# Optimization experiments

Measured on AMD Instinct MI355X. Metric: run time of the kernel, lower is better.

Reference implementation:

```python
import jax, jax.numpy as jnp
import numpy as np

G = 50000            # number of 5-node crystal graphs
NPG = 5              # nodes per graph (forward reshapes to (-1, 5, F))
N = G * NPG          # total nodes
IN = 64              # in_size (61 atomic-number feats + 3 position)
OUT = 64             # out_size
HID = 2 * OUT        # hidden width per __init__


def setup_inputs() -> dict:
    key = jax.random.key(0)
    ks = jax.random.split(key, 8)
    h = jax.random.normal(ks[0], (N, IN - 3), jnp.float32)
    x = jax.random.normal(ks[1], (N, 3), jnp.float32)
    # complete graph with self-loops inside each 5-node crystal
    base = np.arange(G, dtype=np.int64) * NPG
    li = np.repeat(np.arange(NPG, dtype=np.int64), NPG)
    lj = np.tile(np.arange(NPG, dtype=np.int64), NPG)
    src = jnp.asarray((base[:, None] + li[None, :]).reshape(-1))
    dst = jnp.asarray((base[:, None] + lj[None, :]).reshape(-1))

    def lin(k, fi, fo):
        return jax.random.normal(k, (fi, fo), jnp.float32) / np.float32(np.sqrt(fi))

    W1 = lin(ks[2], IN, HID);  b1 = jnp.zeros((HID,), jnp.float32)
    W2 = lin(ks[3], HID, HID); b2 = jnp.zeros((HID,), jnp.float32)
    W3 = lin(ks[4], HID, HID); b3 = jnp.zeros((HID,), jnp.float32)
    W4 = lin(ks[5], HID, OUT); b4 = jnp.zeros((OUT,), jnp.float32)
    return {"h": h, "x": x, "src": src, "dst": dst,
            "W1": W1, "b1": b1, "W2": W2, "b2": b2,
            "W3": W3, "b3": b3, "W4": W4, "b4": b4}


def _graph_conv(feat, src, dst, W, b):
    # DGL GraphConv, norm='both': D_dst^{-1/2} A D_src^{-1/2} X W + b
    e = src.shape[0]
    ones = jnp.ones((e,), feat.dtype)
    deg_out = jax.ops.segment_sum(ones, src, num_segments=N)
    deg_in = jax.ops.segment_sum(ones, dst, num_segments=N)
    norm_src = jax.lax.rsqrt(jnp.maximum(deg_out, 1.0))
    norm_dst = jax.lax.rsqrt(jnp.maximum(deg_in, 1.0))
    norm_e = norm_src[src] * norm_dst[dst]                      # [E]
    agg = jax.ops.segment_sum(feat[src] * norm_e[:, None], dst,
                              num_segments=N)                   # [N, F]
    return agg @ W + b


def reference(h, x, src, dst, W1, b1, W2, b2, W3, b3, W4, b4):
    hx = jnp.concatenate([h, x.astype(jnp.float32)], axis=1)   # [N, IN]
    f1 = _graph_conv(hx, src, dst, W1, b1)
    f2 = _graph_conv(f1, src, dst, W2, b2)
    f3 = _graph_conv(f2, src, dst, W3, b3)
    f4 = _graph_conv(f3, src, dst, W4, b4)                      # [N, OUT]
    return jnp.mean(f4.reshape((-1, NPG, f4.shape[-1])), axis=1)  # [G, OUT]
```

## Files before the change

### kernel.cpp

```cpp
#include <hip/hip_runtime.h>


#define GB 16

__global__ void __launch_bounds__(256) collapse1(
    const float* __restrict__ W1, const float* __restrict__ b1,
    const float* __restrict__ W2, const float* __restrict__ b2,
    const float* __restrict__ W3, const float* __restrict__ b3,
    const float* __restrict__ W4, const float* __restrict__ b4,
    float* __restrict__ ws) {
  __shared__ __align__(16) float smem[128 * 128 + 512];
  int tid = threadIdx.x;
  int bx = blockIdx.x;

  if (bx < 32) {
    float* W2s = smem;
    float* w1s = smem + 16384;
    int i0 = bx * 2;
    {
      const float4* s = (const float4*)W2;
      float4* d = (float4*)W2s;
      #pragma unroll
      for (int j = 0; j < 16; ++j) d[tid + 256 * j] = s[tid + 256 * j];
      if (tid < 64) ((float4*)w1s)[tid] = ((const float4*)(W1 + i0 * 128))[tid];
    }
    __syncthreads();
    int il = tid >> 7, oo = tid & 127;
    float s0 = 0.f, s1 = 0.f, s2 = 0.f, s3 = 0.f;
    #pragma unroll 8
    for (int k = 0; k < 128; k += 4) {
      s0 += w1s[il * 128 + k + 0] * W2s[(k + 0) * 128 + oo];
      s1 += w1s[il * 128 + k + 1] * W2s[(k + 1) * 128 + oo];
      s2 += w1s[il * 128 + k + 2] * W2s[(k + 2) * 128 + oo];
      s3 += w1s[il * 128 + k + 3] * W2s[(k + 3) * 128 + oo];
    }
    ws[(i0 + il) * 128 + oo] = (s0 + s1) + (s2 + s3);
    if (bx == 0 && tid < 128) {
      float s = b2[tid];
      #pragma unroll 4
      for (int k = 0; k < 128; ++k) s += b1[k] * W2s[k * 128 + tid];
      ws[16384 + tid] = s;
    }
  } else {
    float* W4s = smem;
    float* w3s = smem + 8192;
    int i0 = (bx - 32) * 4;
    {
      const float4* s = (const float4*)W4;
      float4* d = (float4*)W4s;
      #pragma unroll
      for (int j = 0; j < 8; ++j) d[tid + 256 * j] = s[tid + 256 * j];
      if (tid < 128) ((float4*)w3s)[tid] = ((const float4*)(W3 + i0 * 128))[tid];
    }
    __syncthreads();
    int il = tid >> 6, o = tid & 63;
    float s0 = 0.f, s1 = 0.f, s2 = 0.f, s3 = 0.f;
    #pragma unroll 8
    for (int k = 0; k < 128; k += 4) {
      s0 += w3s[il * 128 + k + 0] * W4s[(k + 0) * 64 + o];
      s1 += w3s[il * 128 + k + 1] * W4s[(k + 1) * 64 + o];
      s2 += w3s[il * 128 + k + 2] * W4s[(k + 2) * 64 + o];
      s3 += w3s[il * 128 + k + 3] * W4s[(k + 3) * 64 + o];
    }
    ws[8192 + (i0 + il) * 64 + o] = (s0 + s1) + (s2 + s3);
    if (bx == 32 && tid < 64) {
      float s = b4[tid];
      #pragma unroll 4
      for (int k = 0; k < 128; ++k) s += b3[k] * W4s[k * 64 + tid];
      ws[16512 + tid] = s;
    }
  }
}

__global__ void __launch_bounds__(256) collapse2(float* __restrict__ ws) {
  __shared__ __align__(16) float smem[128 * 64 + 512];
  float* Bms = smem;
  float* As  = smem + 8192;
  int tid = threadIdx.x;
  int i0 = blockIdx.x * 4;
  {
    const float4* s = (const float4*)(ws + 8192);
    float4* d = (float4*)Bms;
    #pragma unroll
    for (int j = 0; j < 8; ++j) d[tid + 256 * j] = s[tid + 256 * j];
    if (tid < 128) ((float4*)As)[tid] = ((const float4*)(ws + i0 * 128))[tid];
  }
  __syncthreads();
  int il = tid >> 6, o = tid & 63;
  float s0 = 0.f, s1 = 0.f, s2 = 0.f, s3 = 0.f;
  #pragma unroll 8
  for (int k = 0; k < 128; k += 4) {
    s0 += As[il * 128 + k + 0] * Bms[(k + 0) * 64 + o];
    s1 += As[il * 128 + k + 1] * Bms[(k + 1) * 64 + o];
    s2 += As[il * 128 + k + 2] * Bms[(k + 2) * 64 + o];
    s3 += As[il * 128 + k + 3] * Bms[(k + 3) * 64 + o];
  }
  ws[16640 + (i0 >> 2) * 256 + o * 4 + il] = ((s0 + s1) + (s2 + s3)) * 0.2f;
  if (blockIdx.x == 0 && tid < 64) {
    float s = ws[16512 + tid];
    #pragma unroll 4
    for (int k = 0; k < 128; ++k) s += ws[16384 + k] * Bms[k * 64 + tid];
    ws[20736 + tid] = s;
  }
}

__global__ void __launch_bounds__(256) gcn_main(
    const float* __restrict__ h, const float* __restrict__ x,
    const float* __restrict__ ws, float* __restrict__ out, int G) {
  __shared__ __align__(16) float m_s[4][4][64];

  int tid = threadIdx.x, wv = tid >> 6, lane = tid & 63;
  long gbase = (long)blockIdx.x * GB + wv * 4;
  if (gbase >= G) return;

  float bco = ws[20736 + lane];

  float sv[4];
  #pragma unroll
  for (int j = 0; j < 4; ++j) {
    long g = gbase + j;
    if (g < G) {
      if (lane < 61) {
        const float* p = h + g * 305 + lane;
        sv[j] = p[0] + p[61] + p[122] + p[183] + p[244];
      } else {
        const float* p = x + g * 15 + (lane - 61);
        sv[j] = p[0] + p[3] + p[6] + p[9] + p[12];
      }
    } else {
      sv[j] = 0.f;
    }
  }
  #pragma unroll
  for (int j = 0; j < 4; ++j) m_s[wv][j][lane] = sv[j];

  {
    const float4* Wg = (const float4*)(ws + 16640);
    const float4* m0 = (const float4*)&m_s[wv][0][0];
    const float4* m1 = (const float4*)&m_s[wv][1][0];
    const float4* m2 = (const float4*)&m_s[wv][2][0];
    const float4* m3 = (const float4*)&m_s[wv][3][0];
    float a0 = bco, a1 = bco, a2 = bco, a3 = bco;
    #pragma unroll 4
    for (int q = 0; q < 16; ++q) {
      float4 w = Wg[q * 64 + lane];
      float4 v0 = m0[q];
      float4 v1 = m1[q];
      float4 v2 = m2[q];
      float4 v3 = m3[q];
      a0 += v0.x * w.x + v0.y * w.y + v0.z * w.z + v0.w * w.w;
      a1 += v1.x * w.x + v1.y * w.y + v1.z * w.z + v1.w * w.w;
      a2 += v2.x * w.x + v2.y * w.y + v2.z * w.z + v2.w * w.w;
      a3 += v3.x * w.x + v3.y * w.y + v3.z * w.z + v3.w * w.w;
    }
    long ob = gbase * 64 + lane;
    if (gbase + 0 < G) out[ob + 0]   = a0;
    if (gbase + 1 < G) out[ob + 64]  = a1;
    if (gbase + 2 < G) out[ob + 128] = a2;
    if (gbase + 3 < G) out[ob + 192] = a3;
  }
}

extern "C" void kernel_launch(void* const* d_in, const int* in_sizes, int n_in,
                              void* d_out, int out_size, void* d_ws, size_t ws_size,
                              hipStream_t stream) {
  const float* h  = (const float*)d_in[0];
  const float* x  = (const float*)d_in[1];
  const float* W1 = (const float*)d_in[4];
  const float* b1 = (const float*)d_in[5];
  const float* W2 = (const float*)d_in[6];
  const float* b2 = (const float*)d_in[7];
  const float* W3 = (const float*)d_in[8];
  const float* b3 = (const float*)d_in[9];
  const float* W4 = (const float*)d_in[10];
  const float* b4 = (const float*)d_in[11];
  float* ws = (float*)d_ws;
  float* out = (float*)d_out;

  int G = in_sizes[0] / 305;

  collapse1<<<64, 256, 0, stream>>>(W1, b1, W2, b2, W3, b3, W4, b4, ws);
  collapse2<<<16, 256, 0, stream>>>(ws);

  int blocks = (G + GB - 1) / GB;
  gcn_main<<<blocks, 256, 0, stream>>>(h, x, ws, out, G);
}
```

Baseline: 38.48 us.

## Fuse weight-collapse kernels into one single-block kernel and unify gather pointer

Replaces the two weight-collapse kernels (64 and 16 blocks) with a single 1024-thread block that computes W1·W2·W3·W4 sequentially in shared memory. This removes one kernel launch and the global-memory round-trip of the intermediate products. The trade-off is that the whole chain of three 128-wide matmuls now runs serially on one CU instead of spread across many. The main kernel's gather also folds the h/x branch into one strided pointer to avoid lane divergence.

```diff
diff --git a/kernel.cpp b/kernel.cpp
--- a/kernel.cpp
+++ b/kernel.cpp
@@ -3,104 +3,125 @@
 
 #define GB 16
 
-__global__ void __launch_bounds__(256) collapse1(
+__global__ void __launch_bounds__(1024) collapse(
     const float* __restrict__ W1, const float* __restrict__ b1,
     const float* __restrict__ W2, const float* __restrict__ b2,
     const float* __restrict__ W3, const float* __restrict__ b3,
     const float* __restrict__ W4, const float* __restrict__ b4,
     float* __restrict__ ws) {
-  __shared__ __align__(16) float smem[128 * 128 + 512];
+  __shared__ __align__(16) float wbuf[128 * 128];
+  __shared__ __align__(16) float A[64 * 128];
+  __shared__ __align__(16) float T[64 * 128];
+  __shared__ float bA[128], bT[128];
   int tid = threadIdx.x;
-  int bx = blockIdx.x;
-
-  if (bx < 32) {
-    float* W2s = smem;
-    float* w1s = smem + 16384;
-    int i0 = bx * 2;
-    {
-      const float4* s = (const float4*)W2;
-      float4* d = (float4*)W2s;
-      #pragma unroll
-      for (int j = 0; j < 16; ++j) d[tid + 256 * j] = s[tid + 256 * j];
-      if (tid < 64) ((float4*)w1s)[tid] = ((const float4*)(W1 + i0 * 128))[tid];
-    }
-    __syncthreads();
-    int il = tid >> 7, oo = tid & 127;
+  int o128 = tid & 127, grp8 = tid >> 7;
+  int o64 = tid & 63,  grp16 = tid >> 6;
+
+  {
+    const float4* s = (const float4*)W2;
+    float4* d = (float4*)wbuf;
+    #pragma unroll
+    for (int r = 0; r < 4; ++r) d[tid + 1024 * r] = s[tid + 1024 * r];
+  }
+  __syncthreads();
+
+  #pragma unroll 2
+  for (int r = 0; r < 8; ++r) {
+    int i = grp8 * 8 + r;
+    const float4* w1r = (const float4*)(W1 + i * 128);
     float s0 = 0.f, s1 = 0.f, s2 = 0.f, s3 = 0.f;
     #pragma unroll 8
+    for (int kq = 0; kq < 32; ++kq) {
+      float4 wv = w1r[kq];
+      s0 += wv.x * wbuf[(kq * 4 + 0) * 128 + o128];
+      s1 += wv.y * wbuf[(kq * 4 + 1) * 128 + o128];
+      s2 += wv.z * wbuf[(kq * 4 + 2) * 128 + o128];
+      s3 += wv.w * wbuf[(kq * 4 + 3) * 128 + o128];
+    }
+    A[i * 128 + o128] = (s0 + s1) + (s2 + s3);
+  }
+  if (tid < 128) {
+    float s0 = b2[tid], s1 = 0.f, s2 = 0.f, s3 = 0.f;
+    #pragma unroll 8
     for (int k = 0; k < 128; k += 4) {
-      s0 += w1s[il * 128 + k + 0] * W2s[(k + 0) * 128 + oo];
-      s1 += w1s[il * 128 + k + 1] * W2s[(k + 1) * 128 + oo];
-      s2 += w1s[il * 128 + k + 2] * W2s[(k + 2) * 128 + oo];
-      s3 += w1s[il * 128 + k + 3] * W2s[(k + 3) * 128 + oo];
-    }
-    ws[(i0 + il) * 128 + oo] = (s0 + s1) + (s2 + s3);
-    if (bx == 0 && tid < 128) {
-      float s = b2[tid];
-      #pragma unroll 4
-      for (int k = 0; k < 128; ++k) s += b1[k] * W2s[k * 128 + tid];
-      ws[16384 + tid] = s;
-    }
-  } else {
-    float* W4s = smem;
-    float* w3s = smem + 8192;
-    int i0 = (bx - 32) * 4;
-    {
-      const float4* s = (const float4*)W4;
-      float4* d = (float4*)W4s;
-      #pragma unroll
-      for (int j = 0; j < 8; ++j) d[tid + 256 * j] = s[tid + 256 * j];
-      if (tid < 128) ((float4*)w3s)[tid] = ((const float4*)(W3 + i0 * 128))[tid];
-    }
-    __syncthreads();
-    int il = tid >> 6, o = tid & 63;
+      s0 += b1[k + 0] * wbuf[(k + 0) * 128 + tid];
+      s1 += b1[k + 1] * wbuf[(k + 1) * 128 + tid];
+      s2 += b1[k + 2] * wbuf[(k + 2) * 128 + tid];
+      s3 += b1[k + 3] * wbuf[(k + 3) * 128 + tid];
+    }
+    bA[tid] = (s0 + s1) + (s2 + s3);
+  }
+  __syncthreads();
+
+  {
+    const float4* s = (const float4*)W3;
+    float4* d = (float4*)wbuf;
+    #pragma unroll
+    for (int r = 0; r < 4; ++r) d[tid + 1024 * r] = s[tid + 1024 * r];
+  }
+  __syncthreads();
+
+  #pragma unroll 2
+  for (int r = 0; r < 8; ++r) {
+    int i = grp8 * 8 + r;
+    const float4* ar = (const float4*)(A + i * 128);
     float s0 = 0.f, s1 = 0.f, s2 = 0.f, s3 = 0.f;
     #pragma unroll 8
+    for (int kq = 0; kq < 32; ++kq) {
+      float4 av = ar[kq];
+      s0 += av.x * wbuf[(kq * 4 + 0) * 128 + o128];
+      s1 += av.y * wbuf[(kq * 4 + 1) * 128 + o128];
+      s2 += av.z * wbuf[(kq * 4 + 2) * 128 + o128];
+      s3 += av.w * wbuf[(kq * 4 + 3) * 128 + o128];
+    }
+    T[i * 128 + o128] = (s0 + s1) + (s2 + s3);
+  }
+  if (tid < 128) {
+    float s0 = b3[tid], s1 = 0.f, s2 = 0.f, s3 = 0.f;
+    #pragma unroll 8
     for (int k = 0; k < 128; k += 4) {
-      s0 += w3s[il * 128 + k + 0] * W4s[(k + 0) * 64 + o];
-      s1 += w3s[il * 128 + k + 1] * W4s[(k + 1) * 64 + o];
-      s2 += w3s[il * 128 + k + 2] * W4s[(k + 2) * 64 + o];
-      s3 += w3s[il * 128 + k + 3] * W4s[(k + 3) * 64 + o];
-    }
-    ws[8192 + (i0 + il) * 64 + o] = (s0 + s1) + (s2 + s3);
-    if (bx == 32 && tid < 64) {
-      float s = b4[tid];
-      #pragma unroll 4
-      for (int k = 0; k < 128; ++k) s += b3[k] * W4s[k * 64 + tid];
-      ws[16512 + tid] = s;
-    }
-  }
-}
-
-__global__ void __launch_bounds__(256) collapse2(float* __restrict__ ws) {
-  __shared__ __align__(16) float smem[128 * 64 + 512];
-  float* Bms = smem;
-  float* As  = smem + 8192;
-  int tid = threadIdx.x;
-  int i0 = blockIdx.x * 4;
-  {
-    const float4* s = (const float4*)(ws + 8192);
-    float4* d = (float4*)Bms;
+      s0 += bA[k + 0] * wbuf[(k + 0) * 128 + tid];
+      s1 += bA[k + 1] * wbuf[(k + 1) * 128 + tid];
+      s2 += bA[k + 2] * wbuf[(k + 2) * 128 + tid];
+      s3 += bA[k + 3] * wbuf[(k + 3) * 128 + tid];
+    }
+    bT[tid] = (s0 + s1) + (s2 + s3);
+  }
+  __syncthreads();
+
+  {
+    const float4* s = (const float4*)W4;
+    float4* d = (float4*)wbuf;
     #pragma unroll
-    for (int j = 0; j < 8; ++j) d[tid + 256 * j] = s[tid + 256 * j];
-    if (tid < 128) ((float4*)As)[tid] = ((const float4*)(ws + i0 * 128))[tid];
-  }
-  __syncthreads();
-  int il = tid >> 6, o = tid & 63;
-  float s0 = 0.f, s1 = 0.f, s2 = 0.f, s3 = 0.f;
-  #pragma unroll 8
-  for (int k = 0; k < 128; k += 4) {
-    s0 += As[il * 128 + k + 0] * Bms[(k + 0) * 64 + o];
-    s1 += As[il * 128 + k + 1] * Bms[(k + 1) * 64 + o];
-    s2 += As[il * 128 + k + 2] * Bms[(k + 2) * 64 + o];
-    s3 += As[il * 128 + k + 3] * Bms[(k + 3) * 64 + o];
-  }
-  ws[16640 + (i0 >> 2) * 256 + o * 4 + il] = ((s0 + s1) + (s2 + s3)) * 0.2f;
-  if (blockIdx.x == 0 && tid < 64) {
-    float s = ws[16512 + tid];
-    #pragma unroll 4
-    for (int k = 0; k < 128; ++k) s += ws[16384 + k] * Bms[k * 64 + tid];
-    ws[20736 + tid] = s;
+    for (int r = 0; r < 2; ++r) d[tid + 1024 * r] = s[tid + 1024 * r];
+  }
+  __syncthreads();
+
+  #pragma unroll
+  for (int r = 0; r < 4; ++r) {
+    int i = grp16 * 4 + r;
+    const float4* tr = (const float4*)(T + i * 128);
+    float s0 = 0.f, s1 = 0.f, s2 = 0.f, s3 = 0.f;
+    #pragma unroll 8
+    for (int kq = 0; kq < 32; ++kq) {
+      float4 tv = tr[kq];
+      s0 += tv.x * wbuf[(kq * 4 + 0) * 64 + o64];
+      s1 += tv.y * wbuf[(kq * 4 + 1) * 64 + o64];
+      s2 += tv.z * wbuf[(kq * 4 + 2) * 64 + o64];
+      s3 += tv.w * wbuf[(kq * 4 + 3) * 64 + o64];
+    }
+    ws[16640 + grp16 * 256 + o64 * 4 + r] = ((s0 + s1) + (s2 + s3)) * 0.2f;
+  }
+  if (tid < 64) {
+    float s0 = b4[tid], s1 = 0.f, s2 = 0.f, s3 = 0.f;
+    #pragma unroll 8
+    for (int k = 0; k < 128; k += 4) {
+      s0 += bT[k + 0] * wbuf[(k + 0) * 64 + tid];
+      s1 += bT[k + 1] * wbuf[(k + 1) * 64 + tid];
+      s2 += bT[k + 2] * wbuf[(k + 2) * 64 + tid];
+      s3 += bT[k + 3] * wbuf[(k + 3) * 64 + tid];
+    }
+    ws[20736 + tid] = (s0 + s1) + (s2 + s3);
   }
 }
 
@@ -114,19 +135,16 @@
   if (gbase >= G) return;
 
   float bco = ws[20736 + lane];
+  bool ish = lane < 61;
+  long st = ish ? 61 : 3;
 
   float sv[4];
   #pragma unroll
   for (int j = 0; j < 4; ++j) {
     long g = gbase + j;
     if (g < G) {
-      if (lane < 61) {
-        const float* p = h + g * 305 + lane;
-        sv[j] = p[0] + p[61] + p[122] + p[183] + p[244];
-      } else {
-        const float* p = x + g * 15 + (lane - 61);
-        sv[j] = p[0] + p[3] + p[6] + p[9] + p[12];
-      }
+      const float* p = ish ? (h + g * 305 + lane) : (x + g * 15 + (lane - 61));
+      sv[j] = p[0] + p[st] + p[2 * st] + p[3 * st] + p[4 * st];
     } else {
       sv[j] = 0.f;
     }
@@ -179,8 +197,7 @@
 
   int G = in_sizes[0] / 305;
 
-  collapse1<<<64, 256, 0, stream>>>(W1, b1, W2, b2, W3, b3, W4, b4, ws);
-  collapse2<<<16, 256, 0, stream>>>(ws);
+  collapse<<<1, 1024, 0, stream>>>(W1, b1, W2, b2, W3, b3, W4, b4, ws);
 
   int blocks = (G + GB - 1) / GB;
   gcn_main<<<blocks, 256, 0, stream>>>(h, x, ws, out, G);
```

Measured after the change: 92.20 us. 140% more time.

## Fuse weight collapse and graph pooling into one cooperative kernel with grid syncs

Applied to the files above, without the earlier changes.

Replaces the three launches (two weight-collapse kernels plus the main kernel) with a single cooperative kernel of 1024 persistent blocks. Each block handles up to four tiles of graphs. The per-graph node sums are loaded into LDS before the first grid sync, so input streaming overlaps the weight-matrix collapse done by the first blocks. Two grid.sync barriers order the collapse stages. This removes launch gaps at the cost of grid-wide barrier latency and larger LDS per block, and it falls back to the old three-kernel path if occupancy is insufficient.

```diff
diff --git a/kernel.cpp b/kernel.cpp
--- a/kernel.cpp
+++ b/kernel.cpp
@@ -1,7 +1,161 @@
 #include <hip/hip_runtime.h>
-
+#include <hip/hip_cooperative_groups.h>
+
+namespace cg = cooperative_groups;
+
+
+#define AOFF   0
+#define BOFF   8192
+#define BT1OFF 16384
+#define D1OFF  16512
+#define WCQOFF 16640
+#define BCOFF  20736
 
 #define GB 16
+#define NB 1024
+#define NSLOT 4
+
+__global__ void __launch_bounds__(256, 4) fused_all(
+    const float* __restrict__ h, const float* __restrict__ x,
+    const float* __restrict__ W1, const float* __restrict__ b1,
+    const float* __restrict__ W2, const float* __restrict__ b2,
+    const float* __restrict__ W3, const float* __restrict__ b3,
+    const float* __restrict__ W4, const float* __restrict__ b4,
+    float* __restrict__ ws, float* __restrict__ out, int G) {
+  __shared__ __align__(16) float m_s[NSLOT][4][4][64];
+  __shared__ __align__(16) float redf[256];
+
+  cg::grid_group grid = cg::this_grid();
+  const int tid = threadIdx.x, bid = blockIdx.x;
+  const int wv = tid >> 6, lane = tid & 63;
+  const int NT = (G + GB - 1) / GB;
+
+  if (bid < 64) {
+    int kh = tid >> 7, o = tid & 127;
+    const float* w1 = W1 + bid * 128 + kh * 64;
+    const float* w2 = W2 + (kh * 64) * 128 + o;
+    float a0 = 0.f, a1 = 0.f, a2 = 0.f, a3 = 0.f;
+    #pragma unroll 8
+    for (int kk = 0; kk < 64; kk += 4) {
+      a0 += w1[kk + 0] * w2[(kk + 0) * 128];
+      a1 += w1[kk + 1] * w2[(kk + 1) * 128];
+      a2 += w1[kk + 2] * w2[(kk + 2) * 128];
+      a3 += w1[kk + 3] * w2[(kk + 3) * 128];
+    }
+    float a = (a0 + a1) + (a2 + a3);
+    if (kh) redf[o] = a;
+    __syncthreads();
+    if (!kh) ws[AOFF + bid * 128 + o] = a + redf[o];
+  } else if (bid < 128) {
+    int row_l = tid >> 7, kh = (tid >> 6) & 1, o = tid & 63;
+    int row = (bid - 64) * 2 + row_l;
+    const float* w3 = W3 + row * 128 + kh * 64;
+    const float* w4 = W4 + (kh * 64) * 64 + o;
+    float a0 = 0.f, a1 = 0.f, a2 = 0.f, a3 = 0.f;
+    #pragma unroll 8
+    for (int kk = 0; kk < 64; kk += 4) {
+      a0 += w3[kk + 0] * w4[(kk + 0) * 64];
+      a1 += w3[kk + 1] * w4[(kk + 1) * 64];
+      a2 += w3[kk + 2] * w4[(kk + 2) * 64];
+      a3 += w3[kk + 3] * w4[(kk + 3) * 64];
+    }
+    float a = (a0 + a1) + (a2 + a3);
+    if (kh) redf[row_l * 64 + o] = a;
+    __syncthreads();
+    if (!kh) ws[BOFF + row * 64 + o] = a + redf[row_l * 64 + o];
+  } else if (bid == 128) {
+    if (tid < 128) {
+      float s = b2[tid];
+      #pragma unroll 4
+      for (int k = 0; k < 128; ++k) s += b1[k] * W2[k * 128 + tid];
+      ws[BT1OFF + tid] = s;
+    } else if (tid < 192) {
+      int o = tid - 128;
+      float s = b4[o];
+      #pragma unroll 4
+      for (int k = 0; k < 128; ++k) s += b3[k] * W4[k * 64 + o];
+      ws[D1OFF + o] = s;
+    }
+  }
+
+  const bool ish = lane < 61;
+  const long st = ish ? 61 : 3;
+  #pragma unroll
+  for (int s = 0; s < NSLOT; ++s) {
+    int ts = bid + s * NB;
+    if (ts < NT) {
+      long gb = (long)ts * GB + (long)wv * 4;
+      #pragma unroll
+      for (int j = 0; j < 4; ++j) {
+        long g = gb + j;
+        float sv = 0.f;
+        if (g < G) {
+          const float* p = ish ? (h + g * 305 + lane) : (x + g * 15 + (lane - 61));
+          sv = p[0] + p[st] + p[2 * st] + p[3 * st] + p[4 * st];
+        }
+        m_s[s][wv][j][lane] = sv;
+      }
+    }
+  }
+
+  grid.sync();
+
+  if (bid < 64) {
+    int kq = tid >> 6, o = tid & 63;
+    const float* arow = ws + AOFF + bid * 128 + kq * 32;
+    const float* bm = ws + BOFF + (kq * 32) * 64 + o;
+    float a0 = 0.f, a1 = 0.f, a2 = 0.f, a3 = 0.f;
+    #pragma unroll 8
+    for (int kk = 0; kk < 32; kk += 4) {
+      a0 += arow[kk + 0] * bm[(kk + 0) * 64];
+      a1 += arow[kk + 1] * bm[(kk + 1) * 64];
+      a2 += arow[kk + 2] * bm[(kk + 2) * 64];
+      a3 += arow[kk + 3] * bm[(kk + 3) * 64];
+    }
+    float a = (a0 + a1) + (a2 + a3);
+    if (kq) redf[kq * 64 + o] = a;
+    __syncthreads();
+    if (!kq) {
+      float t = a + redf[64 + o] + redf[128 + o] + redf[192 + o];
+      ws[WCQOFF + (bid >> 2) * 256 + o * 4 + (bid & 3)] = t * 0.2f;
+    }
+  } else if (bid == 64 && tid < 64) {
+    float s = ws[D1OFF + tid];
+    #pragma unroll 4
+    for (int k = 0; k < 128; ++k) s += ws[BT1OFF + k] * ws[BOFF + k * 64 + tid];
+    ws[BCOFF + tid] = s;
+  }
+
+  grid.sync();
+
+  float bco = ws[BCOFF + lane];
+  const float4* Wg = (const float4*)(ws + WCQOFF);
+  #pragma unroll 1
+  for (int s = 0; s < NSLOT; ++s) {
+    int ts = bid + s * NB;
+    if (ts >= NT) break;
+    long gb = (long)ts * GB + (long)wv * 4;
+    const float4* m0 = (const float4*)&m_s[s][wv][0][0];
+    const float4* m1 = (const float4*)&m_s[s][wv][1][0];
+    const float4* m2 = (const float4*)&m_s[s][wv][2][0];
+    const float4* m3 = (const float4*)&m_s[s][wv][3][0];
+    float a0 = bco, a1 = bco, a2 = bco, a3 = bco;
+    #pragma unroll 4
+    for (int q = 0; q < 16; ++q) {
+      float4 w = Wg[q * 64 + lane];
+      float4 v0 = m0[q], v1 = m1[q], v2 = m2[q], v3 = m3[q];
+      a0 += v0.x * w.x + v0.y * w.y + v0.z * w.z + v0.w * w.w;
+      a1 += v1.x * w.x + v1.y * w.y + v1.z * w.z + v1.w * w.w;
+      a2 += v2.x * w.x + v2.y * w.y + v2.z * w.z + v2.w * w.w;
+      a3 += v3.x * w.x + v3.y * w.y + v3.z * w.z + v3.w * w.w;
+    }
+    long ob = gb * 64 + lane;
+    if (gb + 0 < G) out[ob + 0]   = a0;
+    if (gb + 1 < G) out[ob + 64]  = a1;
+    if (gb + 2 < G) out[ob + 128] = a2;
+    if (gb + 3 < G) out[ob + 192] = a3;
+  }
+}
 
 __global__ void __launch_bounds__(256) collapse1(
     const float* __restrict__ W1, const float* __restrict__ b1,
@@ -12,7 +166,6 @@
   __shared__ __align__(16) float smem[128 * 128 + 512];
   int tid = threadIdx.x;
   int bx = blockIdx.x;
-
   if (bx < 32) {
     float* W2s = smem;
     float* w1s = smem + 16384;
@@ -39,7 +192,7 @@
       float s = b2[tid];
       #pragma unroll 4
       for (int k = 0; k < 128; ++k) s += b1[k] * W2s[k * 128 + tid];
-      ws[16384 + tid] = s;
+      ws[BT1OFF + tid] = s;
     }
   } else {
     float* W4s = smem;
@@ -62,12 +215,12 @@
       s2 += w3s[il * 128 + k + 2] * W4s[(k + 2) * 64 + o];
       s3 += w3s[il * 128 + k + 3] * W4s[(k + 3) * 64 + o];
     }
-    ws[8192 + (i0 + il) * 64 + o] = (s0 + s1) + (s2 + s3);
+    ws[BOFF + (i0 + il) * 64 + o] = (s0 + s1) + (s2 + s3);
     if (bx == 32 && tid < 64) {
       float s = b4[tid];
       #pragma unroll 4
       for (int k = 0; k < 128; ++k) s += b3[k] * W4s[k * 64 + tid];
-      ws[16512 + tid] = s;
+      ws[D1OFF + tid] = s;
     }
   }
 }
@@ -79,7 +232,7 @@
   int tid = threadIdx.x;
   int i0 = blockIdx.x * 4;
   {
-    const float4* s = (const float4*)(ws + 8192);
+    const float4* s = (const float4*)(ws + BOFF);
     float4* d = (float4*)Bms;
     #pragma unroll
     for (int j = 0; j < 8; ++j) d[tid + 256 * j] = s[tid + 256 * j];
@@ -95,12 +248,12 @@
     s2 += As[il * 128 + k + 2] * Bms[(k + 2) * 64 + o];
     s3 += As[il * 128 + k + 3] * Bms[(k + 3) * 64 + o];
   }
-  ws[16640 + (i0 >> 2) * 256 + o * 4 + il] = ((s0 + s1) + (s2 + s3)) * 0.2f;
+  ws[WCQOFF + (i0 >> 2) * 256 + o * 4 + il] = ((s0 + s1) + (s2 + s3)) * 0.2f;
   if (blockIdx.x == 0 && tid < 64) {
-    float s = ws[16512 + tid];
+    float s = ws[D1OFF + tid];
     #pragma unroll 4
-    for (int k = 0; k < 128; ++k) s += ws[16384 + k] * Bms[k * 64 + tid];
-    ws[20736 + tid] = s;
+    for (int k = 0; k < 128; ++k) s += ws[BT1OFF + k] * ws[BOFF + k * 64 + tid];
+    ws[BCOFF + tid] = s;
   }
 }
 
@@ -108,34 +261,25 @@
     const float* __restrict__ h, const float* __restrict__ x,
     const float* __restrict__ ws, float* __restrict__ out, int G) {
   __shared__ __align__(16) float m_s[4][4][64];
-
   int tid = threadIdx.x, wv = tid >> 6, lane = tid & 63;
-  long gbase = (long)blockIdx.x * GB + wv * 4;
+  long gbase = (long)blockIdx.x * GB + (long)wv * 4;
   if (gbase >= G) return;
-
-  float bco = ws[20736 + lane];
-
+  float bco = ws[BCOFF + lane];
+  bool ish = lane < 61;
+  long st = ish ? 61 : 3;
   float sv[4];
   #pragma unroll
   for (int j = 0; j < 4; ++j) {
     long g = gbase + j;
     if (g < G) {
-      if (lane < 61) {
-        const float* p = h + g * 305 + lane;
-        sv[j] = p[0] + p[61] + p[122] + p[183] + p[244];
-      } else {
-        const float* p = x + g * 15 + (lane - 61);
-        sv[j] = p[0] + p[3] + p[6] + p[9] + p[12];
-      }
-    } else {
-      sv[j] = 0.f;
-    }
+      const float* p = ish ? (h + g * 305 + lane) : (x + g * 15 + (lane - 61));
+      sv[j] = p[0] + p[st] + p[2 * st] + p[3 * st] + p[4 * st];
+    } else sv[j] = 0.f;
   }
   #pragma unroll
   for (int j = 0; j < 4; ++j) m_s[wv][j][lane] = sv[j];
-
   {
-    const float4* Wg = (const float4*)(ws + 16640);
+    const float4* Wg = (const float4*)(ws + WCQOFF);
     const float4* m0 = (const float4*)&m_s[wv][0][0];
     const float4* m1 = (const float4*)&m_s[wv][1][0];
     const float4* m2 = (const float4*)&m_s[wv][2][0];
@@ -144,10 +288,7 @@
     #pragma unroll 4
     for (int q = 0; q < 16; ++q) {
       float4 w = Wg[q * 64 + lane];
-      float4 v0 = m0[q];
-      float4 v1 = m1[q];
-      float4 v2 = m2[q];
-      float4 v3 = m3[q];
+      float4 v0 = m0[q], v1 = m1[q], v2 = m2[q], v3 = m3[q];
       a0 += v0.x * w.x + v0.y * w.y + v0.z * w.z + v0.w * w.w;
       a1 += v1.x * w.x + v1.y * w.y + v1.z * w.z + v1.w * w.w;
       a2 += v2.x * w.x + v2.y * w.y + v2.z * w.z + v2.w * w.w;
@@ -176,12 +317,24 @@
   const float* b4 = (const float*)d_in[11];
   float* ws = (float*)d_ws;
   float* out = (float*)d_out;
-
   int G = in_sizes[0] / 305;
 
-  collapse1<<<64, 256, 0, stream>>>(W1, b1, W2, b2, W3, b3, W4, b4, ws);
-  collapse2<<<16, 256, 0, stream>>>(ws);
-
-  int blocks = (G + GB - 1) / GB;
-  gcn_main<<<blocks, 256, 0, stream>>>(h, x, ws, out, G);
-}
+  int maxB = 0;
+  hipError_t qe = hipOccupancyMaxActiveBlocksPerMultiprocessor(&maxB, fused_all, 256, 0);
+  bool coop = (qe == hipSuccess && maxB >= 4);
+
+  if (coop) {
+    void* params[] = {(void*)&h, (void*)&x,
+                      (void*)&W1, (void*)&b1, (void*)&W2, (void*)&b2,
+                      (void*)&W3, (void*)&b3, (void*)&W4, (void*)&b4,
+                      (void*)&ws, (void*)&out, (void*)&G};
+    hipError_t le = hipLaunchCooperativeKernel(fused_all, dim3(NB), dim3(256),
+                                               params, 0, stream);
+    if (le != hipSuccess) coop = false;
+  }
+  if (!coop) {
+    collapse1<<<64, 256, 0, stream>>>(W1, b1, W2, b2, W3, b3, W4, b4, ws);
+    collapse2<<<16, 256, 0, stream>>>(ws);
+    gcn_main<<<(G + GB - 1) / GB, 256, 0, stream>>>(h, x, ws, out, G);
+  }
+}
```

Measured after the change: 40.43 us. 5.1% more time.

## Fuse weight-collapse kernels into one row-chained kernel, dropping a launch

Applied to the files above, without the earlier changes.

Replaces the two weight-collapse kernels with one kernel in which each block carries a single W1 row through W2, W3 and W4 in sequence. Partial sums are reduced across wavefronts in shared memory, and one extra block chains the biases. This removes a kernel launch and the intermediate products written to and read back from the workspace. In exchange, each block re-reads W2, W3 and W4 from global memory without shared-memory staging, which adds redundant L2 traffic. The main kernel also merges its h/x load branch into a single strided-pointer path.

```diff
diff --git a/kernel.cpp b/kernel.cpp
--- a/kernel.cpp
+++ b/kernel.cpp
@@ -1,106 +1,93 @@
 #include <hip/hip_runtime.h>
 
 
+#define WCQOFF 16640
+#define BCOFF  20736
 #define GB 16
 
-__global__ void __launch_bounds__(256) collapse1(
+__global__ void __launch_bounds__(256) collapseX(
     const float* __restrict__ W1, const float* __restrict__ b1,
     const float* __restrict__ W2, const float* __restrict__ b2,
     const float* __restrict__ W3, const float* __restrict__ b3,
     const float* __restrict__ W4, const float* __restrict__ b4,
     float* __restrict__ ws) {
-  __shared__ __align__(16) float smem[128 * 128 + 512];
-  int tid = threadIdx.x;
-  int bx = blockIdx.x;
+  __shared__ float red[512];
+  __shared__ float arow[128];
+  __shared__ float trow[128];
 
-  if (bx < 32) {
-    float* W2s = smem;
-    float* w1s = smem + 16384;
-    int i0 = bx * 2;
+  const int tid = threadIdx.x, wv = tid >> 6, lane = tid & 63;
+  const int r = blockIdx.x;
+
+  if (r < 64) {
     {
-      const float4* s = (const float4*)W2;
-      float4* d = (float4*)W2s;
-      #pragma unroll
-      for (int j = 0; j < 16; ++j) d[tid + 256 * j] = s[tid + 256 * j];
-      if (tid < 64) ((float4*)w1s)[tid] = ((const float4*)(W1 + i0 * 128))[tid];
+      const int kb = wv * 32;
+      const float* w1p = W1 + r * 128 + kb;
+      const float* w2p = W2 + kb * 128;
+      float p0 = 0.f, p1 = 0.f;
+      #pragma unroll 8
+      for (int kk = 0; kk < 32; ++kk) {
+        float w1 = w1p[kk];
+        p0 += w1 * w2p[kk * 128 + lane];
+        p1 += w1 * w2p[kk * 128 + lane + 64];
+      }
+      red[wv * 128 + lane] = p0;
+      red[wv * 128 + lane + 64] = p1;
     }
     __syncthreads();
-    int il = tid >> 7, oo = tid & 127;
-    float s0 = 0.f, s1 = 0.f, s2 = 0.f, s3 = 0.f;
-    #pragma unroll 8
-    for (int k = 0; k < 128; k += 4) {
-      s0 += w1s[il * 128 + k + 0] * W2s[(k + 0) * 128 + oo];
-      s1 += w1s[il * 128 + k + 1] * W2s[(k + 1) * 128 + oo];
-      s2 += w1s[il * 128 + k + 2] * W2s[(k + 2) * 128 + oo];
-      s3 += w1s[il * 128 + k + 3] * W2s[(k + 3) * 128 + oo];
+    if (tid < 128) arow[tid] = red[tid] + red[128 + tid] + red[256 + tid] + red[384 + tid];
+    __syncthreads();
+
+    {
+      const int kb = wv * 32;
+      const float* w3p = W3 + kb * 128;
+      float p0 = 0.f, p1 = 0.f;
+      #pragma unroll 8
+      for (int kk = 0; kk < 32; ++kk) {
+        float a = arow[kb + kk];
+        p0 += a * w3p[kk * 128 + lane];
+        p1 += a * w3p[kk * 128 + lane + 64];
+      }
+      red[wv * 128 + lane] = p0;
+      red[wv * 128 + lane + 64] = p1;
     }
-    ws[(i0 + il) * 128 + oo] = (s0 + s1) + (s2 + s3);
-    if (bx == 0 && tid < 128) {
+    __syncthreads();
+    if (tid < 128) trow[tid] = red[tid] + red[128 + tid] + red[256 + tid] + red[384 + tid];
+    __syncthreads();
+
+    {
+      const int kb = wv * 32;
+      const float* w4p = W4 + kb * 64;
+      float p = 0.f;
+      #pragma unroll 8
+      for (int kk = 0; kk < 32; ++kk) p += trow[kb + kk] * w4p[kk * 64 + lane];
+      red[wv * 128 + lane] = p;
+    }
+    __syncthreads();
+    if (tid < 64) {
+      float wc = red[tid] + red[128 + tid] + red[256 + tid] + red[384 + tid];
+      ws[WCQOFF + (r >> 2) * 256 + tid * 4 + (r & 3)] = wc * 0.2f;
+    }
+  } else {
+    if (tid < 128) {
       float s = b2[tid];
       #pragma unroll 4
-      for (int k = 0; k < 128; ++k) s += b1[k] * W2s[k * 128 + tid];
-      ws[16384 + tid] = s;
-    }
-  } else {
-    float* W4s = smem;
-    float* w3s = smem + 8192;
-    int i0 = (bx - 32) * 4;
-    {
-      const float4* s = (const float4*)W4;
-      float4* d = (float4*)W4s;
-      #pragma unroll
-      for (int j = 0; j < 8; ++j) d[tid + 256 * j] = s[tid + 256 * j];
-      if (tid < 128) ((float4*)w3s)[tid] = ((const float4*)(W3 + i0 * 128))[tid];
+      for (int k = 0; k < 128; ++k) s += b1[k] * W2[k * 128 + tid];
+      arow[tid] = s;
     }
     __syncthreads();
-    int il = tid >> 6, o = tid & 63;
-    float s0 = 0.f, s1 = 0.f, s2 = 0.f, s3 = 0.f;
-    #pragma unroll 8
-    for (int k = 0; k < 128; k += 4) {
-      s0 += w3s[il * 128 + k + 0] * W4s[(k + 0) * 64 + o];
-      s1 += w3s[il * 128 + k + 1] * W4s[(k + 1) * 64 + o];
-      s2 += w3s[il * 128 + k + 2] * W4s[(k + 2) * 64 + o];
-      s3 += w3s[il * 128 + k + 3] * W4s[(k + 3) * 64 + o];
+    if (tid < 128) {
+      float s = b3[tid];
+      #pragma unroll 4
+      for (int k = 0; k < 128; ++k) s += arow[k] * W3[k * 128 + tid];
+      trow[tid] = s;
     }
-    ws[8192 + (i0 + il) * 64 + o] = (s0 + s1) + (s2 + s3);
-    if (bx == 32 && tid < 64) {
+    __syncthreads();
+    if (tid < 64) {
       float s = b4[tid];
       #pragma unroll 4
-      for (int k = 0; k < 128; ++k) s += b3[k] * W4s[k * 64 + tid];
-      ws[16512 + tid] = s;
+      for (int k = 0; k < 128; ++k) s += trow[k] * W4[k * 64 + tid];
+      ws[BCOFF + tid] = s;
     }
-  }
-}
-
-__global__ void __launch_bounds__(256) collapse2(float* __restrict__ ws) {
-  __shared__ __align__(16) float smem[128 * 64 + 512];
-  float* Bms = smem;
-  float* As  = smem + 8192;
-  int tid = threadIdx.x;
-  int i0 = blockIdx.x * 4;
-  {
-    const float4* s = (const float4*)(ws + 8192);
-    float4* d = (float4*)Bms;
-    #pragma unroll
-    for (int j = 0; j < 8; ++j) d[tid + 256 * j] = s[tid + 256 * j];
-    if (tid < 128) ((float4*)As)[tid] = ((const float4*)(ws + i0 * 128))[tid];
-  }
-  __syncthreads();
-  int il = tid >> 6, o = tid & 63;
-  float s0 = 0.f, s1 = 0.f, s2 = 0.f, s3 = 0.f;
-  #pragma unroll 8
-  for (int k = 0; k < 128; k += 4) {
-    s0 += As[il * 128 + k + 0] * Bms[(k + 0) * 64 + o];
-    s1 += As[il * 128 + k + 1] * Bms[(k + 1) * 64 + o];
-    s2 += As[il * 128 + k + 2] * Bms[(k + 2) * 64 + o];
-    s3 += As[il * 128 + k + 3] * Bms[(k + 3) * 64 + o];
-  }
-  ws[16640 + (i0 >> 2) * 256 + o * 4 + il] = ((s0 + s1) + (s2 + s3)) * 0.2f;
-  if (blockIdx.x == 0 && tid < 64) {
-    float s = ws[16512 + tid];
-    #pragma unroll 4
-    for (int k = 0; k < 128; ++k) s += ws[16384 + k] * Bms[k * 64 + tid];
-    ws[20736 + tid] = s;
   }
 }
 
@@ -110,32 +97,27 @@
   __shared__ __align__(16) float m_s[4][4][64];
 
   int tid = threadIdx.x, wv = tid >> 6, lane = tid & 63;
-  long gbase = (long)blockIdx.x * GB + wv * 4;
+  long gbase = (long)blockIdx.x * GB + (long)wv * 4;
   if (gbase >= G) return;
 
-  float bco = ws[20736 + lane];
+  float bco = ws[BCOFF + lane];
+  bool ish = lane < 61;
+  long st = ish ? 61 : 3;
 
   float sv[4];
   #pragma unroll
   for (int j = 0; j < 4; ++j) {
     long g = gbase + j;
     if (g < G) {
-      if (lane < 61) {
-        const float* p = h + g * 305 + lane;
-        sv[j] = p[0] + p[61] + p[122] + p[183] + p[244];
-      } else {
-        const float* p = x + g * 15 + (lane - 61);
-        sv[j] = p[0] + p[3] + p[6] + p[9] + p[12];
-      }
-    } else {
-      sv[j] = 0.f;
-    }
+      const float* p = ish ? (h + g * 305 + lane) : (x + g * 15 + (lane - 61));
+      sv[j] = p[0] + p[st] + p[2 * st] + p[3 * st] + p[4 * st];
+    } else sv[j] = 0.f;
   }
   #pragma unroll
   for (int j = 0; j < 4; ++j) m_s[wv][j][lane] = sv[j];
 
   {
-    const float4* Wg = (const float4*)(ws + 16640);
+    const float4* Wg = (const float4*)(ws + WCQOFF);
     const float4* m0 = (const float4*)&m_s[wv][0][0];
     const float4* m1 = (const float4*)&m_s[wv][1][0];
     const float4* m2 = (const float4*)&m_s[wv][2][0];
@@ -144,10 +126,7 @@
     #pragma unroll 4
     for (int q = 0; q < 16; ++q) {
       float4 w = Wg[q * 64 + lane];
-      float4 v0 = m0[q];
-      float4 v1 = m1[q];
-      float4 v2 = m2[q];
-      float4 v3 = m3[q];
+      float4 v0 = m0[q], v1 = m1[q], v2 = m2[q], v3 = m3[q];
       a0 += v0.x * w.x + v0.y * w.y + v0.z * w.z + v0.w * w.w;
       a1 += v1.x * w.x + v1.y * w.y + v1.z * w.z + v1.w * w.w;
       a2 += v2.x * w.x + v2.y * w.y + v2.z * w.z + v2.w * w.w;
@@ -179,9 +158,6 @@
 
   int G = in_sizes[0] / 305;
 
-  collapse1<<<64, 256, 0, stream>>>(W1, b1, W2, b2, W3, b3, W4, b4, ws);
-  collapse2<<<16, 256, 0, stream>>>(ws);
-
-  int blocks = (G + GB - 1) / GB;
-  gcn_main<<<blocks, 256, 0, stream>>>(h, x, ws, out, G);
+  collapseX<<<65, 256, 0, stream>>>(W1, b1, W2, b2, W3, b3, W4, b4, ws);
+  gcn_main<<<(G + GB - 1) / GB, 256, 0, stream>>>(h, x, ws, out, G);
 }
```

Measured after the change: 38.06 us. About the same (-1.1%).
